# Performance work log

Measured on AMD Instinct MI355X. Metric: run time of the kernel, lower is better.

## Reference

```python
import jax, jax.numpy as jnp
import numpy as np

# PyG ChebConv defaults: normalization='sym', lambda_max=2.0.
# L_hat = 2*L/lambda_max - I = (I - D^-1/2 A D^-1/2) - I = -D^-1/2 A D^-1/2
# (self-loop/diagonal coefficient is exactly 0 when lambda_max == 2).

N_NODES = 30000
IN_CH = 128
HID_CH = 256
K = 3
N_EDGES = 480000


def _norm_weights(edge_index, n):
    src, dst = edge_index[0], edge_index[1]
    mask = src != dst  # remove_self_loops
    ones = jnp.where(mask, 1.0, 0.0)
    deg = jax.ops.segment_sum(ones, src, num_segments=n)
    dis = jnp.where(deg > 0, deg ** -0.5, 0.0)  # deg_inv_sqrt, inf -> 0
    w = jnp.where(mask, -dis[src] * dis[dst], 0.0)  # -A_sym edge weights
    return src, dst, w


def _cheb_conv(x, src, dst, w, W, b, n):
    # Tx_0 = x; Tx_1 = L_hat x; Tx_k = 2 L_hat Tx_{k-1} - Tx_{k-2}
    def lap(h):  # sparse matvec: (L_hat h)[i] = sum_{e: dst_e=i} w_e * h[src_e]
        return jax.ops.segment_sum(w[:, None] * h[src], dst, num_segments=n)

    Tx_prev = x
    out = x @ W[0]
    if W.shape[0] > 1:
        Tx_cur = lap(x)
        out = out + Tx_cur @ W[1]
        for k in range(2, W.shape[0]):
            Tx_next = 2.0 * lap(Tx_cur) - Tx_prev
            out = out + Tx_next @ W[k]
            Tx_prev, Tx_cur = Tx_cur, Tx_next
    return out + b


def setup_inputs() -> dict:
    key = jax.random.key(0)
    k1, k2, k3, k4, k5, k6 = jax.random.split(key, 6)
    x = jax.random.normal(k1, (N_NODES, IN_CH), dtype=jnp.float32)
    edge_index = jax.random.randint(k2, (2, N_EDGES), 0, N_NODES, dtype=jnp.int64)
    s1 = (1.0 / (IN_CH * K)) ** 0.5
    s2 = (1.0 / (HID_CH * K)) ** 0.5
    W1 = jax.random.uniform(k3, (K, IN_CH, HID_CH), jnp.float32, -s1, s1)
    b1 = jax.random.uniform(k4, (HID_CH,), jnp.float32, -s1, s1)
    W2 = jax.random.uniform(k5, (K, HID_CH, IN_CH), jnp.float32, -s2, s2)
    b2 = jax.random.uniform(k6, (IN_CH,), jnp.float32, -s2, s2)
    return {"x": x, "edge_index": edge_index, "W1": W1, "b1": b1, "W2": W2, "b2": b2}


def reference(x, edge_index, W1, b1, W2, b2):
    n = x.shape[0]
    src, dst, w = _norm_weights(edge_index, n)
    h = jax.nn.relu(_cheb_conv(x, src, dst, w, W1, b1, n))
    return _cheb_conv(h, src, dst, w, W2, b2, n)
```

## Files before the change

### kernel.cpp

```cpp
#include <hip/hip_runtime.h>
#include <hip/hip_bf16.h>


#define ELLW 64

typedef short bf16x8_t __attribute__((ext_vector_type(8)));
typedef unsigned short u16x4_t __attribute__((ext_vector_type(4)));
typedef unsigned short u16x8_t __attribute__((ext_vector_type(8)));
typedef float f32x4_t __attribute__((ext_vector_type(4)));

static __device__ inline unsigned short f2bf(float f) {
    __hip_bfloat16 h = __float2bfloat16(f);
    return __builtin_bit_cast(unsigned short, h);
}
static __device__ inline float bfbits2f(unsigned int lo16) {
    unsigned int u = lo16 << 16;
    return __builtin_bit_cast(float, u);
}

__global__ __launch_bounds__(256) void build_kernel(const int* __restrict__ src,
                                                    const int* __restrict__ dst,
                                                    int* __restrict__ degi,
                                                    int* __restrict__ cnt,
                                                    unsigned short* __restrict__ ell,
                                                    int E) {
    int e = blockIdx.x * 256 + threadIdx.x;
    if (e >= E) return;
    int s = src[e], d = dst[e];
    if (s != d) atomicAdd(&degi[s], 1);
    int pos = atomicAdd(&cnt[d], 1);
    if (pos < ELLW) ell[(size_t)d * ELLW + pos] = (unsigned short)s;
}

__global__ __launch_bounds__(256) void prep_kernel(const float* __restrict__ W1,
                                                   const float* __restrict__ W2,
                                                   const float* __restrict__ x,
                                                   unsigned short* __restrict__ Bt1,
                                                   unsigned short* __restrict__ Bt2,
                                                   unsigned short* __restrict__ xb,
                                                   int nx4) {
    const int NB1 = 256 * 384, NB2 = 384 * 256;
    int i = blockIdx.x * 256 + threadIdx.x;
    if (i < NB1) {
        int n = i / 384, k = i % 384;
        Bt1[(size_t)n * 384 + k] = f2bf(W1[(size_t)k * 256 + n]);
    } else if (i < NB1 + NB2) {
        int j = i - NB1;
        int n = j / 256, k = j % 256;
        float v;
        if (n < 128) v = W2[(size_t)(1 * 256 + k) * 128 + n];
        else if (n < 256) v = W2[(size_t)(2 * 256 + k) * 128 + (n - 128)];
        else v = W2[(size_t)k * 128 + (n - 256)] - W2[(size_t)(2 * 256 + k) * 128 + (n - 256)];
        Bt2[(size_t)n * 256 + k] = f2bf(v);
    } else {
        int j = i - NB1 - NB2;
        if (j < nx4) {
            f32x4_t v = *(const f32x4_t*)&x[(size_t)j * 4];
            u16x4_t u;
            u.x = f2bf(v.x); u.y = f2bf(v.y); u.z = f2bf(v.z); u.w = f2bf(v.w);
            *(u16x4_t*)&xb[(size_t)j * 4] = u;
        }
    }
}

__global__ __launch_bounds__(256) void lap_ell_kernel(const unsigned short* __restrict__ Xb,
                                                      float* __restrict__ Yf,
                                                      unsigned short* __restrict__ Yb,
                                                      const int* __restrict__ cnt,
                                                      const unsigned short* __restrict__ ell,
                                                      const int* __restrict__ degi,
                                                      const unsigned short* __restrict__ add,
                                                      const float* __restrict__ bias,
                                                      float s, float a, int N) {
    int wave = threadIdx.x >> 6;
    int lane = threadIdx.x & 63;
    int node = blockIdx.x * 4 + wave;
    if (node >= N) return;
    int n = cnt[node];
    if (n > ELLW) n = ELLW;
    int dn = degi[node];
    float fdn = (float)dn;
    const u16x8_t* rows = (const u16x8_t*)(ell + (size_t)node * ELLW);

    float ax[8], ay[8];
#pragma unroll
    for (int k = 0; k < 8; ++k) { ax[k] = 0.0f; ay[k] = 0.0f; }

    int nIter = (n + 7) >> 3;
    for (int t = 0; t < nIter; ++t) {
        u16x8_t s8 = rows[t];
        int base = t * 8;
#pragma unroll
        for (int k = 0; k < 8; ++k) {
            int raw = (int)s8[k];
            int sk = (base + k < n) ? raw : node;
            sk = __builtin_amdgcn_readfirstlane(sk);
            unsigned int v = *(const unsigned int*)&Xb[(size_t)sk * 128 + lane * 2];
            int dsk = degi[sk];
            float wk = (sk != node && dn > 0 && dsk > 0)
                           ? -rsqrtf(fdn * (float)dsk) : 0.0f;
            ax[k] = fmaf(wk, bfbits2f(v & 0xffffu), ax[k]);
            ay[k] = fmaf(wk, bfbits2f(v >> 16), ay[k]);
        }
    }
    float rx = s * (((ax[0] + ax[1]) + (ax[2] + ax[3])) +
                    ((ax[4] + ax[5]) + (ax[6] + ax[7])));
    float ry = s * (((ay[0] + ay[1]) + (ay[2] + ay[3])) +
                    ((ay[4] + ay[5]) + (ay[6] + ay[7])));
    size_t o = (size_t)node * 128 + lane * 2;
    if (add) {
        unsigned int ad = *(const unsigned int*)&add[o];
        rx = fmaf(a, bfbits2f(ad & 0xffffu), rx);
        ry = fmaf(a, bfbits2f(ad >> 16), ry);
    }
    if (bias) {
        rx += bias[lane * 2];
        ry += bias[lane * 2 + 1];
    }
    if (Yf) {
        float2 r; r.x = rx; r.y = ry;
        *(float2*)&Yf[o] = r;
    }
    if (Yb) {
        unsigned int ob = ((unsigned int)f2bf(ry) << 16) | f2bf(rx);
        *(unsigned int*)&Yb[o] = ob;
    }
}

__global__ __launch_bounds__(512) void gemm_mfma_kernel(
        const unsigned short* __restrict__ A0, const unsigned short* __restrict__ A1,
        const unsigned short* __restrict__ A2, int ldA,
        const unsigned short* __restrict__ Bt, int K,
        unsigned short* __restrict__ Ob0, unsigned short* __restrict__ Ob1,
        unsigned short* __restrict__ Ob2,
        int ldO, const float* __restrict__ bias, int M, int relu) {
    __shared__ unsigned short As[128][72];
    __shared__ unsigned short Bs[64][72];

    int tid = threadIdx.x;
    int lane = tid & 63;
    int wid = tid >> 6;
    int wm = wid >> 1;
    int wn = wid & 1;
    int lm = lane & 15, lg = lane >> 4;

    int rowBase = blockIdx.x * 128;
    int colBase = blockIdx.y * 64;

    f32x4_t acc[2][2] = {};

    for (int k0 = 0; k0 < K; k0 += 64) {
        int seg = k0 >> 7;
        int acol = k0 & 127;
        const unsigned short* A = (seg == 0) ? A0 : ((seg == 1) ? A1 : A2);

        {
            int row = tid >> 2;
            int c = (tid & 3) * 16;
            int gr = rowBase + row;
            u16x8_t v0 = {0, 0, 0, 0, 0, 0, 0, 0};
            u16x8_t v1 = {0, 0, 0, 0, 0, 0, 0, 0};
            if (gr < M) {
                const unsigned short* ap = &A[(size_t)gr * ldA + acol + c];
                v0 = *(const u16x8_t*)ap;
                v1 = *(const u16x8_t*)(ap + 8);
            }
            *(u16x8_t*)&As[row][c] = v0;
            *(u16x8_t*)&As[row][c + 8] = v1;
        }
        {
            int n = tid >> 3;
            int kb = tid & 7;
            u16x8_t bv = *(const u16x8_t*)&Bt[(size_t)(colBase + n) * K + k0 + kb * 8];
            *(u16x8_t*)&Bs[n][kb * 8] = bv;
        }
        __syncthreads();

#pragma unroll
        for (int ks = 0; ks < 2; ++ks) {
            int koff = ks * 32 + lg * 8;
            bf16x8_t a0 = *(const bf16x8_t*)&As[wm * 32 + lm][koff];
            bf16x8_t a1 = *(const bf16x8_t*)&As[wm * 32 + 16 + lm][koff];
            bf16x8_t b0 = *(const bf16x8_t*)&Bs[wn * 32 + lm][koff];
            bf16x8_t b1 = *(const bf16x8_t*)&Bs[wn * 32 + 16 + lm][koff];
            acc[0][0] = __builtin_amdgcn_mfma_f32_16x16x32_bf16(a0, b0, acc[0][0], 0, 0, 0);
            acc[0][1] = __builtin_amdgcn_mfma_f32_16x16x32_bf16(a0, b1, acc[0][1], 0, 0, 0);
            acc[1][0] = __builtin_amdgcn_mfma_f32_16x16x32_bf16(a1, b0, acc[1][0], 0, 0, 0);
            acc[1][1] = __builtin_amdgcn_mfma_f32_16x16x32_bf16(a1, b1, acc[1][1], 0, 0, 0);
        }
        __syncthreads();
    }

    int oseg = colBase >> 7;
    unsigned short* Ob = (oseg == 0) ? Ob0 : ((oseg == 1) ? Ob1 : Ob2);
    int lcbase = (colBase & 127) + wn * 32;
#pragma unroll
    for (int i = 0; i < 2; ++i) {
#pragma unroll
        for (int j = 0; j < 2; ++j) {
            int lc = lcbase + j * 16 + lm;
            int gcol = colBase + wn * 32 + j * 16 + lm;
            float bval = bias ? bias[gcol] : 0.0f;
#pragma unroll
            for (int r = 0; r < 4; ++r) {
                int gr = rowBase + wm * 32 + i * 16 + lg * 4 + r;
                if (gr < M) {
                    float v = acc[i][j][r] + bval;
                    if (relu) v = fmaxf(v, 0.0f);
                    Ob[(size_t)gr * ldO + lc] = f2bf(v);
                }
            }
        }
    }
}

extern "C" void kernel_launch(void* const* d_in, const int* in_sizes, int n_in,
                              void* d_out, int out_size, void* d_ws, size_t ws_size,
                              hipStream_t stream) {
    const float* x  = (const float*)d_in[0];
    const int*   ei = (const int*)d_in[1];
    const float* W1 = (const float*)d_in[2];
    const float* b1 = (const float*)d_in[3];
    const float* W2 = (const float*)d_in[4];
    const float* b2 = (const float*)d_in[5];
    float* out = (float*)d_out;

    const int IN = 128, HID = 256;
    int N = in_sizes[0] / IN;
    int E = in_sizes[1] / 2;
    const int* src = ei;
    const int* dst = ei + E;

    char* ws = (char*)d_ws;
    size_t off = 0;
    auto alloc = [&](size_t bytes) -> void* {
        void* p = ws + off;
        off += (bytes + 255) & ~(size_t)255;
        return p;
    };
    int* ibuf   = (int*)alloc((size_t)2 * N * 4);
    int* degi   = ibuf;
    int* cnt    = ibuf + N;
    unsigned short* ell = (unsigned short*)alloc((size_t)N * ELLW * 2);
    unsigned short* xb  = (unsigned short*)alloc((size_t)N * IN * 2);
    unsigned short* T1b = (unsigned short*)alloc((size_t)N * IN * 2);
    unsigned short* T2b = (unsigned short*)alloc((size_t)N * IN * 2);
    unsigned short* A2b = (unsigned short*)alloc((size_t)N * IN * 2);
    unsigned short* Ib  = (unsigned short*)alloc((size_t)N * IN * 2);
    unsigned short* hb  = (unsigned short*)alloc((size_t)N * HID * 2);
    unsigned short* Db  = (unsigned short*)alloc((size_t)N * IN * 2);
    unsigned short* Zb  = (unsigned short*)alloc((size_t)N * IN * 2);
    unsigned short* Bt1 = (unsigned short*)alloc((size_t)256 * 384 * 2);
    unsigned short* Bt2 = (unsigned short*)alloc((size_t)384 * 256 * 2);

    int gLap = (N + 3) / 4;
    int gBlkM = (N + 127) / 128;
    int nx4 = N * IN / 4;
    int prepItems = 256 * 384 + 384 * 256 + nx4;

    hipMemsetAsync(ibuf, 0, (size_t)2 * N * 4, stream);
    build_kernel<<<(E + 255) / 256, 256, 0, stream>>>(src, dst, degi, cnt, ell, E);
    prep_kernel<<<(prepItems + 255) / 256, 256, 0, stream>>>(W1, W2, x, Bt1, Bt2, xb, nx4);

    lap_ell_kernel<<<gLap, 256, 0, stream>>>(xb, nullptr, T1b, cnt, ell, degi,
                                             nullptr, nullptr, 1.0f, 0.0f, N);
    lap_ell_kernel<<<gLap, 256, 0, stream>>>(T1b, nullptr, T2b, cnt, ell, degi,
                                             xb, nullptr, 2.0f, -1.0f, N);
    {
        dim3 grid(gBlkM, 4);
        gemm_mfma_kernel<<<grid, 512, 0, stream>>>(xb, T1b, T2b, IN,
                                                   Bt1, 384,
                                                   hb, hb + 128, nullptr,
                                                   HID, b1, N, 1);
    }

    {
        dim3 grid(gBlkM, 6);
        gemm_mfma_kernel<<<grid, 512, 0, stream>>>(hb, hb + 128, nullptr, HID,
                                                   Bt2, 256,
                                                   Db, A2b, Zb,
                                                   IN, nullptr, N, 0);
        lap_ell_kernel<<<gLap, 256, 0, stream>>>(A2b, nullptr, Ib, cnt, ell, degi,
                                                 Db, nullptr, 2.0f, 1.0f, N);
        lap_ell_kernel<<<gLap, 256, 0, stream>>>(Ib, out, nullptr, cnt, ell, degi,
                                                 Zb, b2, 1.0f, 1.0f, N);
    }
}
```

Measured before the change: 215.4 us.

## Split Laplacian SpMM across half-waves and column halves with 4-way unroll

The ELL SpMM kernel now assigns each node to a 32-lane half-wave covering 64 columns, with a second grid dimension splitting the 128 feature columns in two. The inner loop reads neighbour indices four at a time and keeps four independent accumulators instead of eight-wide padded iterations, dropping the readfirstlane scalarisation and the padding to multiples of eight. This is meant to add parallelism and memory-level concurrency for the gather. In exchange the index row and degree loads are repeated for each column half, and gather accesses become 128-byte segments per half-wave.

```diff
diff --git a/kernel.cpp b/kernel.cpp
--- a/kernel.cpp
+++ b/kernel.cpp
@@ -72,50 +72,65 @@
                                                       const unsigned short* __restrict__ add,
                                                       const float* __restrict__ bias,
                                                       float s, float a, int N) {
-    int wave = threadIdx.x >> 6;
-    int lane = threadIdx.x & 63;
-    int node = blockIdx.x * 4 + wave;
+    int tid = threadIdx.x;
+    int wave = tid >> 6;
+    int lane = tid & 63;
+    int sub = lane >> 5;
+    int l32 = lane & 31;
+    int node = blockIdx.x * 8 + wave * 2 + sub;
     if (node >= N) return;
+    int col = blockIdx.y * 64 + l32 * 2;
+
     int n = cnt[node];
     if (n > ELLW) n = ELLW;
     int dn = degi[node];
     float fdn = (float)dn;
-    const u16x8_t* rows = (const u16x8_t*)(ell + (size_t)node * ELLW);
-
-    float ax[8], ay[8];
-#pragma unroll
-    for (int k = 0; k < 8; ++k) { ax[k] = 0.0f; ay[k] = 0.0f; }
-
-    int nIter = (n + 7) >> 3;
-    for (int t = 0; t < nIter; ++t) {
-        u16x8_t s8 = rows[t];
-        int base = t * 8;
-#pragma unroll
-        for (int k = 0; k < 8; ++k) {
-            int raw = (int)s8[k];
-            int sk = (base + k < n) ? raw : node;
-            sk = __builtin_amdgcn_readfirstlane(sk);
-            unsigned int v = *(const unsigned int*)&Xb[(size_t)sk * 128 + lane * 2];
-            int dsk = degi[sk];
-            float wk = (sk != node && dn > 0 && dsk > 0)
-                           ? -rsqrtf(fdn * (float)dsk) : 0.0f;
-            ax[k] = fmaf(wk, bfbits2f(v & 0xffffu), ax[k]);
-            ay[k] = fmaf(wk, bfbits2f(v >> 16), ay[k]);
-        }
-    }
-    float rx = s * (((ax[0] + ax[1]) + (ax[2] + ax[3])) +
-                    ((ax[4] + ax[5]) + (ax[6] + ax[7])));
-    float ry = s * (((ay[0] + ay[1]) + (ay[2] + ay[3])) +
-                    ((ay[4] + ay[5]) + (ay[6] + ay[7])));
-    size_t o = (size_t)node * 128 + lane * 2;
+    const unsigned short* row = ell + (size_t)node * ELLW;
+    const unsigned short* Xc = Xb + col;
+
+    float ax0 = 0.f, ay0 = 0.f, ax1 = 0.f, ay1 = 0.f;
+    float ax2 = 0.f, ay2 = 0.f, ax3 = 0.f, ay3 = 0.f;
+    int j = 0;
+    for (; j + 4 <= n; j += 4) {
+        u16x4_t s4 = *(const u16x4_t*)&row[j];
+        int s0 = (int)s4.x, s1 = (int)s4.y, s2 = (int)s4.z, s3 = (int)s4.w;
+        unsigned int v0 = *(const unsigned int*)&Xc[(size_t)s0 * 128];
+        unsigned int v1 = *(const unsigned int*)&Xc[(size_t)s1 * 128];
+        unsigned int v2 = *(const unsigned int*)&Xc[(size_t)s2 * 128];
+        unsigned int v3 = *(const unsigned int*)&Xc[(size_t)s3 * 128];
+        int d0 = degi[s0], d1 = degi[s1], d2 = degi[s2], d3 = degi[s3];
+        float w0 = (s0 != node && dn > 0 && d0 > 0) ? -rsqrtf(fdn * (float)d0) : 0.0f;
+        float w1 = (s1 != node && dn > 0 && d1 > 0) ? -rsqrtf(fdn * (float)d1) : 0.0f;
+        float w2 = (s2 != node && dn > 0 && d2 > 0) ? -rsqrtf(fdn * (float)d2) : 0.0f;
+        float w3 = (s3 != node && dn > 0 && d3 > 0) ? -rsqrtf(fdn * (float)d3) : 0.0f;
+        ax0 = fmaf(w0, bfbits2f(v0 & 0xffffu), ax0);
+        ay0 = fmaf(w0, bfbits2f(v0 >> 16), ay0);
+        ax1 = fmaf(w1, bfbits2f(v1 & 0xffffu), ax1);
+        ay1 = fmaf(w1, bfbits2f(v1 >> 16), ay1);
+        ax2 = fmaf(w2, bfbits2f(v2 & 0xffffu), ax2);
+        ay2 = fmaf(w2, bfbits2f(v2 >> 16), ay2);
+        ax3 = fmaf(w3, bfbits2f(v3 & 0xffffu), ax3);
+        ay3 = fmaf(w3, bfbits2f(v3 >> 16), ay3);
+    }
+    for (; j < n; ++j) {
+        int s0 = (int)row[j];
+        unsigned int v0 = *(const unsigned int*)&Xc[(size_t)s0 * 128];
+        int d0 = degi[s0];
+        float w0 = (s0 != node && dn > 0 && d0 > 0) ? -rsqrtf(fdn * (float)d0) : 0.0f;
+        ax0 = fmaf(w0, bfbits2f(v0 & 0xffffu), ax0);
+        ay0 = fmaf(w0, bfbits2f(v0 >> 16), ay0);
+    }
+    float rx = s * ((ax0 + ax1) + (ax2 + ax3));
+    float ry = s * ((ay0 + ay1) + (ay2 + ay3));
+    size_t o = (size_t)node * 128 + col;
     if (add) {
         unsigned int ad = *(const unsigned int*)&add[o];
         rx = fmaf(a, bfbits2f(ad & 0xffffu), rx);
         ry = fmaf(a, bfbits2f(ad >> 16), ry);
     }
     if (bias) {
-        rx += bias[lane * 2];
-        ry += bias[lane * 2 + 1];
+        rx += bias[col];
+        ry += bias[col + 1];
     }
     if (Yf) {
         float2 r; r.x = rx; r.y = ry;
@@ -253,7 +268,7 @@
     unsigned short* Bt1 = (unsigned short*)alloc((size_t)256 * 384 * 2);
     unsigned short* Bt2 = (unsigned short*)alloc((size_t)384 * 256 * 2);
 
-    int gLap = (N + 3) / 4;
+    dim3 gLap((N + 7) / 8, 2);
     int gBlkM = (N + 127) / 128;
     int nx4 = N * IN / 4;
     int prepItems = 256 * 384 + 384 * 256 + nx4;
```

After: 229.3 us. +6.5%, slower.
